# Optimization experiments

Hardware: AMD Instinct MI355X
Metric: run time of the kernel (lower is better)

Reference implementation:

```python
import jax, jax.numpy as jnp
import numpy as np

B, S, D, H = 4, 2048, 768, 12
DEPTH = D // H


def setup_inputs() -> dict:
    key = jax.random.key(0)
    ks = jax.random.split(key, 8)
    scale = 1.0 / np.sqrt(D)
    inp = {
        "q": jax.random.normal(ks[0], (B, S, D), jnp.float32),
        "k": jax.random.normal(ks[1], (B, S, D), jnp.float32),
        "v": jax.random.normal(ks[2], (B, S, D), jnp.float32),
        # additive mask: 1.0 at disallowed (future) positions, causal
        "mask": jnp.triu(jnp.ones((S, S), jnp.float32), k=1)[None, None, :, :],
        "wq": jax.random.normal(ks[3], (D, D), jnp.float32) * scale,
        "wk": jax.random.normal(ks[4], (D, D), jnp.float32) * scale,
        "wv": jax.random.normal(ks[5], (D, D), jnp.float32) * scale,
        "w_dense": jax.random.normal(ks[6], (D, D), jnp.float32) * scale,
        "b_dense": jnp.zeros((D,), jnp.float32),
    }
    return inp


def _split_heads(x):
    b, s, _ = x.shape
    return x.reshape(b, s, H, DEPTH).transpose(0, 2, 1, 3)  # [B,H,S,depth]


def reference(q, k, v, mask, wq, wk, wv, w_dense, b_dense):
    qh = _split_heads(q @ wq.T)
    kh = _split_heads(k @ wk.T)
    vh = _split_heads(v @ wv.T)
    scale = jnp.sqrt(jnp.float32(DEPTH))
    logits = jnp.einsum("bhqd,bhkd->bhqk", qh, kh) / scale  # [B,H,S,S]
    logits = logits + mask * -1e9
    attn = jax.nn.softmax(logits, axis=-1)
    out = jnp.einsum("bhqk,bhkd->bhqd", attn, vh)
    out = out.transpose(0, 2, 1, 3).reshape(q.shape[0], -1, D)
    return out @ w_dense.T + b_dense
```

## Files before the change

### kernel.cpp

```cpp
#include <hip/hip_runtime.h>

typedef __attribute__((ext_vector_type(8))) short short8;
typedef __attribute__((ext_vector_type(4))) float f32x4;
typedef __attribute__((ext_vector_type(4))) unsigned int uint4v;

static __device__ __forceinline__ unsigned pack2(float x, float y) {
  unsigned ux = __float_as_uint(x) + 0x8000u;
  unsigned uy = __float_as_uint(y) + 0x8000u;
  return __builtin_amdgcn_perm(uy, ux, 0x07060302u);
}
static __device__ __forceinline__ unsigned packt(float x, float y) {
  return __builtin_amdgcn_perm(__float_as_uint(y), __float_as_uint(x), 0x07060302u);
}

#define GLDS(g, l)                                                                     \
  __builtin_amdgcn_global_load_lds((const __attribute__((address_space(1))) void*)(g), \
                                   (__attribute__((address_space(3))) void*)(l), 16, 0, 0)

__global__ __launch_bounds__(256) void cvt_all(const float* __restrict__ q,
                                               const float* __restrict__ k,
                                               const float* __restrict__ v,
                                               const float* __restrict__ w0,
                                               const float* __restrict__ w1,
                                               const float* __restrict__ w2,
                                               const float* __restrict__ w3,
                                               unsigned short* __restrict__ oq,
                                               unsigned short* __restrict__ ok,
                                               unsigned short* __restrict__ ov,
                                               unsigned short* __restrict__ o0,
                                               unsigned short* __restrict__ o1,
                                               unsigned short* __restrict__ o2,
                                               unsigned short* __restrict__ o3) {
  const int bx = blockIdx.x;
  const float* s;
  unsigned short* d;
  long i;
  if (bx < 18432) {
    int seg = bx / 6144;
    s = seg == 0 ? q : seg == 1 ? k : v;
    d = seg == 0 ? oq : seg == 1 ? ok : ov;
    i = (long)(bx - seg * 6144) * 256 + threadIdx.x;
  } else {
    int t = bx - 18432;
    int seg = t / 576;
    s = seg == 0 ? w0 : seg == 1 ? w1 : seg == 2 ? w2 : w3;
    d = seg == 0 ? o0 : seg == 1 ? o1 : seg == 2 ? o2 : o3;
    i = (long)(t - seg * 576) * 256 + threadIdx.x;
  }
  float4 val = ((const float4*)s)[i];
  uint2 o;
  o.x = pack2(val.x, val.y);
  o.y = pack2(val.z, val.w);
  *(uint2*)(d + 4 * i) = o;
}

template <int MODE>
static __device__ __forceinline__ void proj_body(const unsigned short* __restrict__ A,
                                                 const unsigned short* __restrict__ W,
                                                 unsigned short* __restrict__ O, int m0,
                                                 int n0, unsigned short* buf,
                                                 float scale) {
  constexpr int K = 768;
  const int tid = threadIdx.x, lane = tid & 63, wave = tid >> 6;
  const int ln = lane & 15, quad = lane >> 4;
  const int wm = (wave & 1) << 6, wn = (wave >> 1) << 6;

  const int o0 = tid << 4, o1 = 4096 + (tid << 4);
  const int cxp = (((tid & 3) ^ ((tid >> 3) & 3)) << 3);
  const unsigned short* gA0 = A + (long)(m0 + (o0 >> 6)) * K + cxp;
  const unsigned short* gA1 = A + (long)(m0 + (o1 >> 6)) * K + cxp;
  const unsigned short* gW0 = W + (long)(n0 + (o0 >> 6)) * K + cxp;
  const unsigned short* gW1 = W + (long)(n0 + (o1 >> 6)) * K + cxp;

  GLDS(gA0, buf + (o0 >> 1));
  GLDS(gA1, buf + (o1 >> 1));
  GLDS(gW0, buf + 8192 + (o0 >> 1));
  GLDS(gW1, buf + 8192 + (o1 >> 1));

  const int qsw = (quad * 8) ^ (((ln >> 1) & 3) << 3);

  f32x4 acc[4][4] = {};
  for (int t = 0; t < 24; t++) {
    const int cur = t & 1, nxt = cur ^ 1;
    const int k1 = (t + 1) << 5;
    __syncthreads();
    if (t < 23) {
      GLDS(gA0 + k1, buf + nxt * 4096 + (o0 >> 1));
      GLDS(gA1 + k1, buf + nxt * 4096 + (o1 >> 1));
      GLDS(gW0 + k1, buf + 8192 + nxt * 4096 + (o0 >> 1));
      GLDS(gW1 + k1, buf + 8192 + nxt * 4096 + (o1 >> 1));
    }
    const unsigned short* As = buf + cur * 4096;
    const unsigned short* Bs = buf + 8192 + cur * 4096;
    short8 af[4], bfr[4];
#pragma unroll
    for (int mi = 0; mi < 4; mi++)
      af[mi] = *(const short8*)(As + (wm + mi * 16 + ln) * 32 + qsw);
#pragma unroll
    for (int ni = 0; ni < 4; ni++)
      bfr[ni] = *(const short8*)(Bs + (wn + ni * 16 + ln) * 32 + qsw);
#pragma unroll
    for (int mi = 0; mi < 4; mi++)
#pragma unroll
      for (int ni = 0; ni < 4; ni++)
        acc[mi][ni] = (MODE == 0)
                          ? __builtin_amdgcn_mfma_f32_16x16x32_bf16(bfr[ni], af[mi],
                                                                    acc[mi][ni], 0, 0, 0)
                          : __builtin_amdgcn_mfma_f32_16x16x32_bf16(af[mi], bfr[ni],
                                                                    acc[mi][ni], 0, 0, 0);
  }

  unsigned short* Ts = buf;
  __syncthreads();
  if (MODE == 0) {
#pragma unroll
    for (int mi = 0; mi < 4; mi++)
#pragma unroll
      for (int ni = 0; ni < 4; ni++) {
        f32x4 v = acc[mi][ni];
        int s = wm + mi * 16 + ln;
        int n = wn + ni * 16 + quad * 4;
        uint2 w2;
        w2.x = pack2(v[0] * scale, v[1] * scale);
        w2.y = pack2(v[2] * scale, v[3] * scale);
        *(uint2*)(Ts + s * 136 + n) = w2;
      }
    __syncthreads();
    const int part = tid & 7, sg0 = tid >> 3;
#pragma unroll
    for (int p = 0; p < 8; p++) {
      int seg = sg0 + p * 32;
      int hh = seg >> 7, s = seg & 127;
      short8 val = *(const short8*)(Ts + s * 136 + hh * 64 + part * 8);
      int gs = m0 + s;
      int bb = gs >> 11, srow = gs & 2047;
      int head = (n0 >> 6) + hh;
      *(short8*)(O + (((long)(bb * 12 + head) * 2048 + srow) << 6) + part * 8) = val;
    }
  } else {
#pragma unroll
    for (int mi = 0; mi < 4; mi++)
#pragma unroll
      for (int ni = 0; ni < 4; ni++) {
        f32x4 v = acc[mi][ni];
        int d = wn + ni * 16 + ln;
        int s = wm + mi * 16 + quad * 4;
        uint2 w2;
        w2.x = pack2(v[0], v[1]);
        w2.y = pack2(v[2], v[3]);
        *(uint2*)(Ts + d * 136 + s) = w2;
      }
    __syncthreads();
    const int part = tid & 15, r0 = tid >> 4;
    const int bb = m0 >> 11, sbase = m0 & 2047;
#pragma unroll
    for (int p = 0; p < 8; p++) {
      int d = r0 + p * 16;
      short8 val = *(const short8*)(Ts + d * 136 + part * 8);
      int head = (n0 >> 6) + (d >> 6);
      int dl = d & 63;
      *(short8*)(O + ((long)(bb * 12 + head) * 64 + dl) * 2048 + sbase + part * 8) = val;
    }
  }
}

__global__ __launch_bounds__(256) void proj_all(
    const unsigned short* __restrict__ qb, const unsigned short* __restrict__ kb,
    const unsigned short* __restrict__ vb, const unsigned short* __restrict__ wq,
    const unsigned short* __restrict__ wk, const unsigned short* __restrict__ wv,
    unsigned short* __restrict__ qh, unsigned short* __restrict__ kh,
    unsigned short* __restrict__ vt) {
  __shared__ unsigned short buf[17408];
  const int bx = blockIdx.x;
  const int xcd = bx & 7;
  const int i = bx >> 3;
  const int op = i / 48, j = i % 48;
  const int m0 = ((j / 6) * 8 + xcd) << 7, n0 = (j % 6) << 7;
  if (op == 0)
    proj_body<0>(qb, wq, qh, m0, n0, buf, 0.18033688011112042f);
  else if (op == 1)
    proj_body<0>(kb, wk, kh, m0, n0, buf, 1.0f);
  else
    proj_body<1>(vb, wv, vt, m0, n0, buf, 1.0f);
}

__global__ __launch_bounds__(256) void dense_gemm(const unsigned short* __restrict__ A,
                                                  const unsigned short* __restrict__ W,
                                                  const float* __restrict__ bias,
                                                  float* __restrict__ out) {
  constexpr int K = 768;
  __shared__ unsigned short buf[16384];
  const int bx = blockIdx.x;
  const int xcd = bx & 7;
  const int i = bx >> 3;
  const int m0 = ((i / 6) * 8 + xcd) << 7;
  const int n0 = (i % 6) << 7;

  const int tid = threadIdx.x, lane = tid & 63, wave = tid >> 6;
  const int ln = lane & 15, quad = lane >> 4;
  const int wm = (wave & 1) << 6, wn = (wave >> 1) << 6;

  const int o0 = tid << 4, o1 = 4096 + (tid << 4);
  const int cxp = (((tid & 3) ^ ((tid >> 3) & 3)) << 3);
  const unsigned short* gA0 = A + (long)(m0 + (o0 >> 6)) * K + cxp;
  const unsigned short* gA1 = A + (long)(m0 + (o1 >> 6)) * K + cxp;
  const unsigned short* gW0 = W + (long)(n0 + (o0 >> 6)) * K + cxp;
  const unsigned short* gW1 = W + (long)(n0 + (o1 >> 6)) * K + cxp;

  GLDS(gA0, buf + (o0 >> 1));
  GLDS(gA1, buf + (o1 >> 1));
  GLDS(gW0, buf + 8192 + (o0 >> 1));
  GLDS(gW1, buf + 8192 + (o1 >> 1));

  const int qsw = (quad * 8) ^ (((ln >> 1) & 3) << 3);

  f32x4 acc[4][4] = {};
  for (int t = 0; t < 24; t++) {
    const int cur = t & 1, nxt = cur ^ 1;
    const int k1 = (t + 1) << 5;
    __syncthreads();
    if (t < 23) {
      GLDS(gA0 + k1, buf + nxt * 4096 + (o0 >> 1));
      GLDS(gA1 + k1, buf + nxt * 4096 + (o1 >> 1));
      GLDS(gW0 + k1, buf + 8192 + nxt * 4096 + (o0 >> 1));
      GLDS(gW1 + k1, buf + 8192 + nxt * 4096 + (o1 >> 1));
    }
    const unsigned short* As = buf + cur * 4096;
    const unsigned short* Bs = buf + 8192 + cur * 4096;
    short8 af[4], bfr[4];
#pragma unroll
    for (int mi = 0; mi < 4; mi++)
      af[mi] = *(const short8*)(As + (wm + mi * 16 + ln) * 32 + qsw);
#pragma unroll
    for (int ni = 0; ni < 4; ni++)
      bfr[ni] = *(const short8*)(Bs + (wn + ni * 16 + ln) * 32 + qsw);
#pragma unroll
    for (int mi = 0; mi < 4; mi++)
#pragma unroll
      for (int ni = 0; ni < 4; ni++)
        acc[mi][ni] =
            __builtin_amdgcn_mfma_f32_16x16x32_bf16(bfr[ni], af[mi], acc[mi][ni], 0, 0, 0);
  }

#pragma unroll
  for (int mi = 0; mi < 4; mi++) {
    const int m = m0 + wm + mi * 16 + ln;
#pragma unroll
    for (int ni = 0; ni < 4; ni++) {
      const int n = n0 + wn + ni * 16 + quad * 4;
      f32x4 v = acc[mi][ni];
      float4 bv = *(const float4*)(bias + n);
      float4 st;
      st.x = v[0] + bv.x;
      st.y = v[1] + bv.y;
      st.z = v[2] + bv.z;
      st.w = v[3] + bv.w;
      *(float4*)(out + (long)m * 768 + n) = st;
    }
  }
}

__global__ __launch_bounds__(256, 3) void attn_kernel(const unsigned short* __restrict__ Qh,
                                                      const unsigned short* __restrict__ Kh,
                                                      const unsigned short* __restrict__ Vt,
                                                      unsigned short* __restrict__ outp) {
  constexpr int S = 2048;
  __shared__ unsigned short sbuf[16384];

  const int bx = blockIdx.x;
  const int xcd = bx & 7;
  const int ii = bx >> 3;
  const int pr = ii & 15, grp = ii >> 4;
  const int bh = grp * 8 + xcd;
  const int h = bh % 12, b = bh / 12;
  const int qtA = pr, qtB = 31 - pr;
  const int tid = threadIdx.x, wave = tid >> 6, lane = tid & 63;
  const int ln = lane & 15, quad = lane >> 4;

  const unsigned short* Qg = Qh + (long)(b * 12 + h) * S * 64;
  const unsigned short* Kg = Kh + (long)(b * 12 + h) * S * 64;
  const unsigned short* Vg = Vt + (long)(b * 12 + h) * 64 * S;

  const int qrA = qtA * 64 + wave * 16 + ln;
  const int qrB = qtB * 64 + wave * 16 + ln;

  short8 bQa0 = *(const short8*)(Qg + qrA * 64 + quad * 8);
  short8 bQa1 = *(const short8*)(Qg + qrA * 64 + 32 + quad * 8);
  short8 bQb0 = *(const short8*)(Qg + qrB * 64 + quad * 8);
  short8 bQb1 = *(const short8*)(Qg + qrB * 64 + 32 + quad * 8);

  float sumA = 0.f, sumB = 0.f;
  f32x4 Oa[4] = {};
  f32x4 Ob[4] = {};
  unsigned pkA[8][2], pkB[8][2];

  const int nkA = (qtA >> 1) + 1;
  const int nkB = (qtB >> 1) + 1;
  const int l0 = ln + ((quad & 1) << 5);
  const bool hi = quad >= 2;

  const int srow = tid >> 2, sc = (tid & 3) << 3;
  const int koff0 = srow * 64 + sc;
  const int koff1 = (srow + 64) * 64 + sc;
  const int koff2 = srow * 64 + 32 + sc;
  const int koff3 = (srow + 64) * 64 + 32 + sc;
  const long voff = (long)srow * 2048 + sc;

  const int wsw = (tid * 8) ^ (((tid >> 3) & 3) << 3);
  const int qsw = (quad * 8) ^ (((ln >> 1) & 3) << 3);

  short8 kc[4], vc[4];
  {
    kc[0] = *(const short8*)(Kg + koff0);
    kc[1] = *(const short8*)(Kg + koff1);
    kc[2] = *(const short8*)(Kg + koff2);
    kc[3] = *(const short8*)(Kg + koff3);
    vc[0] = *(const short8*)(Vg + voff);
    vc[1] = *(const short8*)(Vg + voff + 32);
    vc[2] = *(const short8*)(Vg + voff + 64);
    vc[3] = *(const short8*)(Vg + voff + 96);
  }

  for (int kt = 0; kt < nkB; kt++) {
    __syncthreads();
    {
      unsigned short* w = sbuf + wsw;
      *(short8*)(w) = kc[0];
      *(short8*)(w + 2048) = kc[1];
      *(short8*)(w + 4096) = kc[2];
      *(short8*)(w + 6144) = kc[3];
      *(short8*)(w + 8192) = vc[0];
      *(short8*)(w + 10240) = vc[1];
      *(short8*)(w + 12288) = vc[2];
      *(short8*)(w + 14336) = vc[3];
    }
    __syncthreads();
    if (kt + 1 < nkB) {
      const unsigned short* kg = Kg + (kt + 1) * 8192;
      const unsigned short* vg = Vg + (kt + 1) * 128;
      kc[0] = *(const short8*)(kg + koff0);
      kc[1] = *(const short8*)(kg + koff1);
      kc[2] = *(const short8*)(kg + koff2);
      kc[3] = *(const short8*)(kg + koff3);
      vc[0] = *(const short8*)(vg + voff);
      vc[1] = *(const short8*)(vg + voff + 32);
      vc[2] = *(const short8*)(vg + voff + 64);
      vc[3] = *(const short8*)(vg + voff + 96);
    }

    const bool actA = kt < nkA;
    const bool dgA = actA && (kt == nkA - 1);
    const bool dgB = (kt == nkB - 1);
    const int limA = actA ? (dgA ? ((qtA & 1) ? 8 : 4) : 8) : 0;
    const int limB = dgB ? ((qtB & 1) ? 8 : 4) : 8;
    const int limQ = limA > limB ? limA : limB;
    const int kbase = kt * 128 + quad * 4;

#pragma unroll
    for (int ni = 0; ni < 8; ni++) {
      if (ni < limQ) {
        const int fro = (ni * 16 + ln) * 32 + qsw;
        short8 k0 = *(const short8*)(sbuf + fro);
        short8 k1 = *(const short8*)(sbuf + 4096 + fro);
        const int key = kbase + ni * 16;
        if (ni < limA) {
          f32x4 s = {};
          s = __builtin_amdgcn_mfma_f32_16x16x32_bf16(k0, bQa0, s, 0, 0, 0);
          s = __builtin_amdgcn_mfma_f32_16x16x32_bf16(k1, bQa1, s, 0, 0, 0);
          float p0 = exp2f(s[0]), p1 = exp2f(s[1]);
          float p2 = exp2f(s[2]), p3 = exp2f(s[3]);
          if (dgA) {
            p0 = (key + 0 > qrA) ? 0.f : p0;
            p1 = (key + 1 > qrA) ? 0.f : p1;
            p2 = (key + 2 > qrA) ? 0.f : p2;
            p3 = (key + 3 > qrA) ? 0.f : p3;
          }
          sumA += (p0 + p1) + (p2 + p3);
          pkA[ni][0] = packt(p0, p1);
          pkA[ni][1] = packt(p2, p3);
        }
        if (ni < limB) {
          f32x4 s = {};
          s = __builtin_amdgcn_mfma_f32_16x16x32_bf16(k0, bQb0, s, 0, 0, 0);
          s = __builtin_amdgcn_mfma_f32_16x16x32_bf16(k1, bQb1, s, 0, 0, 0);
          float p0 = exp2f(s[0]), p1 = exp2f(s[1]);
          float p2 = exp2f(s[2]), p3 = exp2f(s[3]);
          if (dgB) {
            p0 = (key + 0 > qrB) ? 0.f : p0;
            p1 = (key + 1 > qrB) ? 0.f : p1;
            p2 = (key + 2 > qrB) ? 0.f : p2;
            p3 = (key + 3 > qrB) ? 0.f : p3;
          }
          sumB += (p0 + p1) + (p2 + p3);
          pkB[ni][0] = packt(p0, p1);
          pkB[ni][1] = packt(p2, p3);
        }
      }
    }

    auto mkB = [&](unsigned (&pk)[8][2], int kk) -> short8 {
      unsigned va0 = (unsigned)__shfl((int)pk[2 * kk][0], l0, 64);
      unsigned vb0 = (unsigned)__shfl((int)pk[2 * kk + 1][0], l0, 64);
      unsigned va1 = (unsigned)__shfl((int)pk[2 * kk][1], l0, 64);
      unsigned vb1 = (unsigned)__shfl((int)pk[2 * kk + 1][1], l0, 64);
      unsigned va2 = (unsigned)__shfl((int)pk[2 * kk][0], l0 + 16, 64);
      unsigned vb2 = (unsigned)__shfl((int)pk[2 * kk + 1][0], l0 + 16, 64);
      unsigned va3 = (unsigned)__shfl((int)pk[2 * kk][1], l0 + 16, 64);
      unsigned vb3 = (unsigned)__shfl((int)pk[2 * kk + 1][1], l0 + 16, 64);
      uint4v tv;
      tv.x = hi ? vb0 : va0;
      tv.y = hi ? vb1 : va1;
      tv.z = hi ? vb2 : va2;
      tv.w = hi ? vb3 : va3;
      return __builtin_bit_cast(short8, tv);
    };

    const int kkA = limA >> 1, kkB = limB >> 1;
#pragma unroll
    for (int kk = 0; kk < 4; kk++) {
      if (kk < kkB) {
        short8 Bb = mkB(pkB, kk);
        short8 Ba;
        if (kk < kkA) Ba = mkB(pkA, kk);
        const unsigned short* vp = sbuf + 8192 + kk * 2048;
#pragma unroll
        for (int di = 0; di < 4; di++) {
          short8 aV = *(const short8*)(vp + (di * 16 + ln) * 32 + qsw);
          Ob[di] = __builtin_amdgcn_mfma_f32_16x16x32_bf16(aV, Bb, Ob[di], 0, 0, 0);
          if (kk < kkA) Oa[di] = __builtin_amdgcn_mfma_f32_16x16x32_bf16(aV, Ba, Oa[di], 0, 0, 0);
        }
      }
    }
  }

  sumA += __shfl_xor(sumA, 16);
  sumA += __shfl_xor(sumA, 32);
  sumB += __shfl_xor(sumB, 16);
  sumB += __shfl_xor(sumB, 32);

  __syncthreads();
  unsigned short* Ts = sbuf;
  {
    float rlA = 1.0f / sumA, rlB = 1.0f / sumB;
    const int row = wave * 16 + ln;
#pragma unroll
    for (int di = 0; di < 4; di++) {
      uint2 wa, wb;
      wa.x = pack2(Oa[di][0] * rlA, Oa[di][1] * rlA);
      wa.y = pack2(Oa[di][2] * rlA, Oa[di][3] * rlA);
      wb.x = pack2(Ob[di][0] * rlB, Ob[di][1] * rlB);
      wb.y = pack2(Ob[di][2] * rlB, Ob[di][3] * rlB);
      *(uint2*)(Ts + row * 72 + di * 16 + quad * 4) = wa;
      *(uint2*)(Ts + (row + 64) * 72 + di * 16 + quad * 4) = wb;
    }
  }
  __syncthreads();
  const int part = tid & 7, r0 = tid >> 3;
#pragma unroll
  for (int p = 0; p < 4; p++) {
    int row = r0 + p * 32;
    int seg = row >> 6, qq = row & 63;
    int qrow = (seg ? qtB : qtA) * 64 + qq;
    short8 val = *(const short8*)(Ts + row * 72 + part * 8);
    *(short8*)(outp + ((long)b * S + qrow) * 768 + h * 64 + part * 8) = val;
  }
}

extern "C" void kernel_launch(void* const* d_in, const int* in_sizes, int n_in,
                              void* d_out, int out_size, void* d_ws, size_t ws_size,
                              hipStream_t stream) {
  const float* q = (const float*)d_in[0];
  const float* k = (const float*)d_in[1];
  const float* v = (const float*)d_in[2];
  const float* wq = (const float*)d_in[4];
  const float* wk = (const float*)d_in[5];
  const float* wv = (const float*)d_in[6];
  const float* wd = (const float*)d_in[7];
  const float* bd = (const float*)d_in[8];
  float* out = (float*)d_out;

  const long QKV = 4L * 2048 * 768;
  const long WN = 768L * 768;
  if (ws_size < (size_t)(7 * QKV + 4 * WN) * 2) return;

  unsigned short* qb = (unsigned short*)d_ws;
  unsigned short* kb = qb + QKV;
  unsigned short* vb = kb + QKV;
  unsigned short* wqb = vb + QKV;
  unsigned short* wkb = wqb + WN;
  unsigned short* wvb = wkb + WN;
  unsigned short* wdb = wvb + WN;
  unsigned short* qh = wdb + WN;
  unsigned short* kh = qh + QKV;
  unsigned short* vt = kh + QKV;
  unsigned short* at = vt + QKV;

  cvt_all<<<20736, 256, 0, stream>>>(q, k, v, wq, wk, wv, wd, qb, kb, vb, wqb, wkb, wvb, wdb);
  proj_all<<<1152, 256, 0, stream>>>(qb, kb, vb, wqb, wkb, wvb, qh, kh, vt);
  attn_kernel<<<768, 256, 0, stream>>>(qh, kh, vt, at);
  dense_gemm<<<384, 256, 0, stream>>>(at, wdb, bd, out);
}
```

Measured before the change: 269.2 us.

## Permute V layout in LDS to drop cross-lane shuffles for P operand

The V tile is now written to shared memory with a key-permuted layout: each thread splits its 8 values into two 4-element halves placed at swizzled offsets. This lets the packed softmax probabilities be used directly as the MFMA B operand with no per-iteration __shfl permutation. It removes 16 cross-lane shuffles and selects per kk step in exchange for narrower 8-byte LDS stores when staging V.

```diff
diff --git a/kernel.cpp b/kernel.cpp
--- a/kernel.cpp
+++ b/kernel.cpp
@@ -296,8 +296,6 @@
 
   const int nkA = (qtA >> 1) + 1;
   const int nkB = (qtB >> 1) + 1;
-  const int l0 = ln + ((quad & 1) << 5);
-  const bool hi = quad >= 2;
 
   const int srow = tid >> 2, sc = (tid & 3) << 3;
   const int koff0 = srow * 64 + sc;
@@ -306,8 +304,12 @@
   const int koff3 = (srow + 64) * 64 + 32 + sc;
   const long voff = (long)srow * 2048 + sc;
 
-  const int wsw = (tid * 8) ^ (((tid >> 3) & 3) << 3);
+  const int swzr = ((tid >> 3) & 3) << 3;
+  const int wsw = (tid * 8) ^ swzr;
   const int qsw = (quad * 8) ^ (((ln >> 1) & 3) << 3);
+  const int vplo = ((((tid & 1) << 4) | ((tid & 2) << 1)) ^ swzr);
+  const int vphi = vplo ^ 8;
+  unsigned short* vwrow = sbuf + 8192 + srow * 32;
 
   short8 kc[4], vc[4];
   {
@@ -329,10 +331,17 @@
       *(short8*)(w + 2048) = kc[1];
       *(short8*)(w + 4096) = kc[2];
       *(short8*)(w + 6144) = kc[3];
-      *(short8*)(w + 8192) = vc[0];
-      *(short8*)(w + 10240) = vc[1];
-      *(short8*)(w + 12288) = vc[2];
-      *(short8*)(w + 14336) = vc[3];
+#pragma unroll
+      for (int c = 0; c < 4; c++) {
+        uint4v vv = __builtin_bit_cast(uint4v, vc[c]);
+        uint2 lo, hi;
+        lo.x = vv.x;
+        lo.y = vv.y;
+        hi.x = vv.z;
+        hi.y = vv.w;
+        *(uint2*)(vwrow + c * 2048 + vplo) = lo;
+        *(uint2*)(vwrow + c * 2048 + vphi) = hi;
+      }
     }
     __syncthreads();
     if (kt + 1 < nkB) {
@@ -398,30 +407,25 @@
       }
     }
 
-    auto mkB = [&](unsigned (&pk)[8][2], int kk) -> short8 {
-      unsigned va0 = (unsigned)__shfl((int)pk[2 * kk][0], l0, 64);
-      unsigned vb0 = (unsigned)__shfl((int)pk[2 * kk + 1][0], l0, 64);
-      unsigned va1 = (unsigned)__shfl((int)pk[2 * kk][1], l0, 64);
-      unsigned vb1 = (unsigned)__shfl((int)pk[2 * kk + 1][1], l0, 64);
-      unsigned va2 = (unsigned)__shfl((int)pk[2 * kk][0], l0 + 16, 64);
-      unsigned vb2 = (unsigned)__shfl((int)pk[2 * kk + 1][0], l0 + 16, 64);
-      unsigned va3 = (unsigned)__shfl((int)pk[2 * kk][1], l0 + 16, 64);
-      unsigned vb3 = (unsigned)__shfl((int)pk[2 * kk + 1][1], l0 + 16, 64);
-      uint4v tv;
-      tv.x = hi ? vb0 : va0;
-      tv.y = hi ? vb1 : va1;
-      tv.z = hi ? vb2 : va2;
-      tv.w = hi ? vb3 : va3;
-      return __builtin_bit_cast(short8, tv);
-    };
-
     const int kkA = limA >> 1, kkB = limB >> 1;
 #pragma unroll
     for (int kk = 0; kk < 4; kk++) {
       if (kk < kkB) {
-        short8 Bb = mkB(pkB, kk);
+        uint4v tb;
+        tb.x = pkB[2 * kk][0];
+        tb.y = pkB[2 * kk][1];
+        tb.z = pkB[2 * kk + 1][0];
+        tb.w = pkB[2 * kk + 1][1];
+        short8 Bb = __builtin_bit_cast(short8, tb);
         short8 Ba;
-        if (kk < kkA) Ba = mkB(pkA, kk);
+        if (kk < kkA) {
+          uint4v ta;
+          ta.x = pkA[2 * kk][0];
+          ta.y = pkA[2 * kk][1];
+          ta.z = pkA[2 * kk + 1][0];
+          ta.w = pkA[2 * kk + 1][1];
+          Ba = __builtin_bit_cast(short8, ta);
+        }
         const unsigned short* vp = sbuf + 8192 + kk * 2048;
 #pragma unroll
         for (int di = 0; di < 4; di++) {
```

After: 261.4 us. 2.9% less time.
